# Optimization experiments

Measured on AMD Instinct MI355X. Metric: run time of the kernel, lower is better.

Reference implementation:

```python
import jax, jax.numpy as jnp
import numpy as np

B, T, C, H = 4, 2048, 2048, 16
D = C // H  # head dim = 128


def setup_inputs() -> dict:
    key = jax.random.key(0)
    k1, k2, k3, k4 = jax.random.split(key, 4)
    x = jax.random.normal(k1, (B, T, C), dtype=jnp.float32)
    # per-token key mask; force token 0 valid so no causal row is fully masked
    tok_mask = jax.random.randint(k2, (B, T), 0, 2).astype(bool).at[:, 0].set(True)
    s = 1.0 / np.sqrt(C).astype(np.float32)
    W_qkv = jax.random.normal(k3, (C, 3 * C), dtype=jnp.float32) * s
    W_proj = jax.random.normal(k4, (C, C), dtype=jnp.float32) * s
    return {"x": x, "tok_mask": tok_mask, "W_qkv": W_qkv, "W_proj": W_proj}


def reference(x, tok_mask, W_qkv, W_proj):
    Bx, Tx, Cx = x.shape
    qkv = x @ W_qkv                              # [B,T,3C]
    q, k, v = jnp.split(qkv, 3, axis=-1)
    q = q.reshape(Bx, Tx, H, D)
    k = k.reshape(Bx, Tx, H, D)
    v = v.reshape(Bx, Tx, H, D)
    scale = 1.0 / np.sqrt(D).astype(np.float32)
    scores = jnp.einsum('bqhd,bkhd->bhqk', q, k) * scale  # [B,H,T,T]
    causal = jnp.tril(jnp.ones((Tx, Tx), dtype=bool))      # [T,T]
    # tok_mask broadcasts over the query dim (key mask), AND-ed with causal
    mask = tok_mask[:, None, :] & causal                   # [B,T,T]
    scores = jnp.where(mask[:, None, :, :], scores, -jnp.inf)
    attn = jax.nn.softmax(scores, axis=-1)                 # dropout p=0 -> identity
    y = jnp.einsum('bhqk,bkhd->bqhd', attn, v).reshape(Bx, Tx, Cx)
    return y @ W_proj
```

## Files before the change

kernel.cpp:

```cpp
#include <hip/hip_runtime.h>
#include <hip/hip_bf16.h>
#include <stdint.h>

typedef __bf16 bf16;
typedef __bf16 bf16x8 __attribute__((ext_vector_type(8)));
typedef __bf16 bf16x4 __attribute__((ext_vector_type(4)));
typedef float f32x4 __attribute__((ext_vector_type(4)));
typedef unsigned short u16;
typedef unsigned int u32;

constexpr int NB = 4;
constexpr int NT = 2048;
constexpr int NC = 2048;
constexpr int NH = 16;
constexpr int ND = 128;
constexpr int NC3 = 6144;

__device__ __forceinline__ void gload16(const void* g, void* l) {
  __builtin_amdgcn_global_load_lds((const __attribute__((address_space(1))) void*)g,
                                   (__attribute__((address_space(3))) void*)l, 16, 0, 0);
}

__device__ __forceinline__ u32 pack_bf16(float a, float b) {
  return (u32)__builtin_bit_cast(u16, (bf16)a) | ((u32)__builtin_bit_cast(u16, (bf16)b) << 16);
}

__global__ __launch_bounds__(256) void ingest_k(const float* __restrict__ raw, bf16* __restrict__ out, long n) {
  long i = ((long)blockIdx.x * 256 + threadIdx.x) * 8;
  if (i >= n) return;
  f32x4 a = *(const f32x4*)(raw + i), b = *(const f32x4*)(raw + i + 4);
  bf16x8 o;
  o[0] = (bf16)a[0]; o[1] = (bf16)a[1]; o[2] = (bf16)a[2]; o[3] = (bf16)a[3];
  o[4] = (bf16)b[0]; o[5] = (bf16)b[1]; o[6] = (bf16)b[2]; o[7] = (bf16)b[3];
  *(bf16x8*)(out + i) = o;
}

__global__ void mask_prep_k(const void* raw, char* out) {
  __shared__ int s_gt1, s_oddnz, s_allb, s_allf, s_allh;
  if (threadIdx.x == 0) { s_gt1 = 0; s_oddnz = 0; s_allb = 1; s_allf = 1; s_allh = 1; }
  __syncthreads();
  const unsigned int* mw = (const unsigned int*)raw;
  int gt1 = 0, oddnz = 0, allb = 1, allf = 1, allh = 1;
  for (int i = threadIdx.x; i < 2048; i += 256) {
    unsigned v = mw[i];
    if (v > 1u) gt1 = 1;
    if ((i & 1) && v) oddnz = 1;
#pragma unroll
    for (int bb = 0; bb < 4; ++bb) { unsigned by = (v >> (8*bb)) & 0xffu; if (by > 1u) allb = 0; }
    if (v != 0u && v != 0x3F800000u) allf = 0;
    unsigned lo = v & 0xffffu, hi = v >> 16;
    if ((lo != 0u && lo != 0x3F80u) || (hi != 0u && hi != 0x3F80u)) allh = 0;
  }
  if (gt1) atomicOr(&s_gt1, 1);
  if (oddnz) atomicOr(&s_oddnz, 1);
  if (!allb) atomicAnd(&s_allb, 0);
  if (!allf) atomicAnd(&s_allf, 0);
  if (!allh) atomicAnd(&s_allh, 0);
  __syncthreads();
  int mode;
  if (!s_gt1)       mode = s_oddnz ? 0 : 2;
  else if (s_allf)  mode = 3;
  else if (s_allb)  mode = 1;
  else if (s_allh)  mode = 4;
  else              mode = 0;
  for (int i = threadIdx.x; i < NB*NT; i += 256) {
    int v;
    if (mode == 0)      v = (((const int*)raw)[i] != 0);
    else if (mode == 1) v = (((const unsigned char*)raw)[i] != 0);
    else if (mode == 2) v = (((const long long*)raw)[i] != 0);
    else if (mode == 3) v = (((const unsigned int*)raw)[i] != 0);
    else                v = (((const unsigned short*)raw)[i] != 0);
    out[i] = (char)v;
  }
}

__global__ __launch_bounds__(256) void transpose_f32_k(const float* __restrict__ in, bf16* __restrict__ out,
                                                       int in_rs, int out_rs) {
  __shared__ __align__(16) bf16 t[64][72];
  const int r0 = blockIdx.y << 6, c0 = blockIdx.x << 6;
  const int tid = threadIdx.x;
#pragma unroll
  for (int i = 0; i < 4; ++i) {
    int slot = i*256 + tid, row = slot >> 4, c4 = slot & 15;
    f32x4 v = *(const f32x4*)(in + (long)(r0 + row)*in_rs + c0 + c4*4);
#pragma unroll
    for (int e = 0; e < 4; ++e) t[c4*4 + e][row] = (bf16)v[e];
  }
  __syncthreads();
#pragma unroll
  for (int i = 0; i < 2; ++i) {
    int slot = i*256 + tid, row = slot >> 3, c8 = slot & 7;
    bf16x8 v = *(const bf16x8*)(&t[row][c8*8]);
    *(bf16x8*)(out + (long)(c0 + row)*out_rs + r0 + c8*8) = v;
  }
}

#define G256_READ_A(qm_) \
  _Pragma("unroll") \
  for (int mi = 0; mi < 4; ++mi) { \
    _Pragma("unroll") \
    for (int kk = 0; kk < 2; ++kk) { \
      const int ri = (qm_)*64 + mi*16 + r; \
      af[mi*2+kk] = *(const bf16x8*)(Ac + wm*16384 + ri*128 + (((kk*4 + g) ^ (ri & 7)) << 4)); \
    } \
  }
#define G256_READ_B(qn_) \
  _Pragma("unroll") \
  for (int ni = 0; ni < 2; ++ni) { \
    _Pragma("unroll") \
    for (int kk = 0; kk < 2; ++kk) { \
      const int ri = (qn_)*32 + ni*16 + r; \
      bfr[ni*2+kk] = *(const bf16x8*)(Bc + wn*8192 + ri*128 + (((kk*4 + g) ^ (ri & 7)) << 4)); \
    } \
  }
#define G256_MFMA(mb_, nb_) \
  __builtin_amdgcn_s_setprio(1); \
  _Pragma("unroll") \
  for (int mi = 0; mi < 4; ++mi) \
    _Pragma("unroll") \
    for (int ni = 0; ni < 2; ++ni) \
      _Pragma("unroll") \
      for (int kk = 0; kk < 2; ++kk) \
        acc[(mb_)+mi][(nb_)+ni] = __builtin_amdgcn_mfma_f32_16x16x32_bf16(af[mi*2+kk], bfr[ni*2+kk], acc[(mb_)+mi][(nb_)+ni], 0, 0, 0); \
  __builtin_amdgcn_s_setprio(0);
#define G256_EDGE(vm_) \
  asm volatile("s_waitcnt vmcnt(" #vm_ ")" ::: "memory"); \
  __builtin_amdgcn_s_barrier(); \
  __builtin_amdgcn_sched_barrier(0);
#define G256_EDGE_NOVM() \
  asm volatile("" ::: "memory"); \
  __builtin_amdgcn_s_barrier(); \
  __builtin_amdgcn_sched_barrier(0);

template <typename OT, bool VTE>
__global__ __launch_bounds__(512, 2) void gemm256_k(const bf16* __restrict__ A, const bf16* __restrict__ BT,
                                                    OT* __restrict__ Cout, int M, int N, int K, int nbx) {
  const int nwg = gridDim.x;
  const int bid = blockIdx.x;
  const int cpx = nwg >> 3;
  const int swz = (bid & 7) * cpx + (bid >> 3);
  const int bx = swz % nbx, by = swz / nbx;
  const long m0 = (long)by << 8, n0 = (long)bx << 8;

  const int tid = threadIdx.x, w = tid >> 6, l = tid & 63, g = l >> 4, r = l & 15;
  const int wm = w >> 2, wn = w & 3;

  __shared__ __align__(16) char As[2][32768];
  __shared__ __align__(16) char Bs[2][32768];

  long aoff2[4], boff2[4];
  int alds[4], blds[4];
#pragma unroll
  for (int i = 0; i < 4; ++i) {
    int s = i*256 + (tid & 255);
    int ri = s >> 3, c = s & 7, cp = c ^ (ri & 7);
    aoff2[i] = (m0 + wm*128 + ri) * (long)K + cp*8;
    alds[i] = wm*16384 + ((i*256 + (w & 3)*64) << 4);
    int s2 = i*128 + wm*64 + l;
    int ri2 = s2 >> 3, c2 = s2 & 7, cp2 = c2 ^ (ri2 & 7);
    boff2[i] = (n0 + wn*64 + ri2) * (long)K + cp2*8;
    blds[i] = wn*8192 + ((i*128 + wm*64) << 4);
  }

  const f32x4 z4 = {0.f, 0.f, 0.f, 0.f};
  f32x4 acc[8][4];
#pragma unroll
  for (int i = 0; i < 8; ++i)
#pragma unroll
    for (int j = 0; j < 4; ++j) acc[i][j] = z4;

  const int nk = K >> 6;
  gload16(A + aoff2[0], As[0] + alds[0]);
  gload16(A + aoff2[1], As[0] + alds[1]);
  gload16(BT + boff2[0], Bs[0] + blds[0]);
  gload16(BT + boff2[1], Bs[0] + blds[1]);
  gload16(A + aoff2[2], As[0] + alds[2]);
  gload16(A + aoff2[3], As[0] + alds[3]);
  gload16(BT + boff2[2], Bs[0] + blds[2]);
  gload16(BT + boff2[3], Bs[0] + blds[3]);
  G256_EDGE(4);

  bf16x8 af[8], bfr[4];

  for (int t = 0; t < nk - 1; ++t) {
    const int cur = t & 1;
    const char* Ac = As[cur];
    const char* Bc = Bs[cur];
    char* An = As[cur ^ 1];
    char* Bn = Bs[cur ^ 1];
    const long ko = (long)(t + 1) << 6;

    G256_READ_A(0); G256_READ_B(0);
    gload16(A + aoff2[0] + ko, An + alds[0]);
    gload16(A + aoff2[1] + ko, An + alds[1]);
    gload16(BT + boff2[0] + ko, Bn + blds[0]);
    gload16(BT + boff2[1] + ko, Bn + blds[1]);
    G256_MFMA(0, 0);
    G256_EDGE(6);

    G256_READ_A(1);
    gload16(A + aoff2[2] + ko, An + alds[2]);
    gload16(A + aoff2[3] + ko, An + alds[3]);
    gload16(BT + boff2[2] + ko, Bn + blds[2]);
    gload16(BT + boff2[3] + ko, Bn + blds[3]);
    G256_MFMA(4, 0);
    G256_EDGE(8);

    G256_READ_B(1);
    G256_MFMA(4, 2);
    G256_EDGE_NOVM();

    G256_READ_A(0);
    G256_MFMA(0, 2);
    G256_EDGE(4);
  }

  {
    const int cur = (nk - 1) & 1;
    const char* Ac = As[cur];
    const char* Bc = Bs[cur];
    G256_READ_A(0); G256_READ_B(0);
    G256_MFMA(0, 0);
    G256_EDGE(2);
    G256_READ_A(1);
    G256_MFMA(4, 0);
    G256_EDGE(0);
    G256_READ_B(1);
    G256_MFMA(4, 2);
    G256_EDGE_NOVM();
    G256_READ_A(0);
    G256_MFMA(0, 2);
  }

  if (VTE && n0 >= 2*NC) {
#pragma unroll
    for (int mi = 0; mi < 8; ++mi)
#pragma unroll
      for (int ni = 0; ni < 4; ++ni) {
        int d_f = (int)(n0 - 2*NC) + wn*64 + ni*16 + r;
        long mr = m0 + wm*128 + mi*16 + 4*g;
        int bb = (int)(mr >> 11), tt = (int)(mr & 2047);
        int hh = d_f >> 7, dd = d_f & 127;
        long rr = (long)(bb*NH + hh)*ND + dd;
        bf16x4 v;
        v[0] = (bf16)acc[mi][ni][0]; v[1] = (bf16)acc[mi][ni][1];
        v[2] = (bf16)acc[mi][ni][2]; v[3] = (bf16)acc[mi][ni][3];
        *(bf16x4*)(Cout + rr*NC3 + 2*NC + tt) = v;
      }
  } else {
#pragma unroll
    for (int mi = 0; mi < 8; ++mi)
#pragma unroll
      for (int ni = 0; ni < 4; ++ni)
#pragma unroll
        for (int j = 0; j < 4; ++j) {
          long mr = m0 + wm*128 + mi*16 + 4*g + j;
          long nc = n0 + wn*64 + ni*16 + r;
          Cout[mr*(long)N + nc] = (OT)acc[mi][ni][j];
        }
  }
}

__global__ __launch_bounds__(256, 2) void attn_k(const bf16* __restrict__ qkv,
                                                 const char* __restrict__ maskC, bf16* __restrict__ y) {
  const int qx = blockIdx.x, h = blockIdx.y, b = blockIdx.z;
  const int qb = (qx & 1) ? (15 - (qx >> 1)) : (qx >> 1);
  const int tid = threadIdx.x, w = tid >> 6, l = tid & 63, g = l >> 4, r = l & 15;
  const int q0 = qb << 7;
  const int bh = b*NH + h;
  const int ntiles = (qb << 1) + 2;
  const int qrowA = q0 + w*32 + r;
  const int qrowB = qrowA + 16;

  __shared__ __align__(16) char Klds[2][16384];
  __shared__ __align__(16) char Vlds[2][16384];
  __shared__ __align__(16) char Plds[8192];
  __shared__ char Mc[2048];
  char* Pl = Plds + (w << 11);

  for (int i = tid; i < q0 + 128; i += 256) Mc[i] = maskC[b*NT + i];

  long koff[4], voff[4];
  int klo[4];
#pragma unroll
  for (int i = 0; i < 4; ++i) {
    int slot = i*256 + tid;
    int row = slot >> 4, c = slot & 15, cp = c ^ (row & 7);
    koff[i] = (long)row*NC3 + cp*8;
    klo[i] = (i*256 + w*64) << 4;
    int vrow = slot >> 3, vc = slot & 7, vcp = vc ^ (vrow & 7);
    voff[i] = (long)vrow*NC3 + vcp*8;
  }
  const bf16* kbase0 = qkv + (long)(b*NT)*NC3 + (NC + h*ND);
  const bf16* vbase0 = qkv + (long)bh*ND*NC3 + 2*NC;

  bf16x8 qfA[4], qfB[4];
  {
    const bf16* qpA = qkv + (long)(b*NT + qrowA)*NC3 + h*ND + g*8;
    const bf16* qpB = qkv + (long)(b*NT + qrowB)*NC3 + h*ND + g*8;
#pragma unroll
    for (int dk = 0; dk < 4; ++dk) {
      qfA[dk] = *(const bf16x8*)(qpA + dk*32);
      qfB[dk] = *(const bf16x8*)(qpB + dk*32);
    }
  }

  const f32x4 z4 = {0.f, 0.f, 0.f, 0.f};
  f32x4 accA[8], accB[8];
#pragma unroll
  for (int i = 0; i < 8; ++i) { accA[i] = z4; accB[i] = z4; }
  float m_runA = 0.0f, l_runA = 0.0f;
  float m_runB = 0.0f, l_runB = 0.0f;

  const float SCL = 0.08838834764831845f * 1.4426950408889634f;

#pragma unroll
  for (int i = 0; i < 4; ++i) {
    gload16(kbase0 + koff[i], Klds[0] + klo[i]);
    gload16(vbase0 + voff[i], Vlds[0] + klo[i]);
  }
  __syncthreads();

  for (int kt = 0; kt < ntiles; ++kt) {
    const int cur = kt & 1;
    if (kt + 1 < ntiles) {
      const bf16* kb = kbase0 + (long)((kt+1)*64)*NC3;
      const bf16* vb = vbase0 + (kt+1)*64;
#pragma unroll
      for (int i = 0; i < 4; ++i) {
        gload16(kb + koff[i], Klds[cur^1] + klo[i]);
        gload16(vb + voff[i], Vlds[cur^1] + klo[i]);
      }
    }
    const char* Kl = Klds[cur];
    const char* Vl = Vlds[cur];
    const int key0 = kt*64;
    const bool actB = (key0 <= q0 + w*32 + 31);
    const bool actA = (key0 <= q0 + w*32 + 15);

    if (actB) {
      u32 mw_[4];
#pragma unroll
      for (int kc = 0; kc < 4; ++kc) mw_[kc] = *(const u32*)(Mc + key0 + kc*16 + 4*g);

      float tvA[4][4], tvB[4][4];
      __builtin_amdgcn_s_setprio(1);
#pragma unroll
      for (int kc = 0; kc < 4; ++kc) {
        const int krow = kc*16 + r;
        bf16x8 kf[4];
#pragma unroll
        for (int dk = 0; dk < 4; ++dk)
          kf[dk] = *(const bf16x8*)(Kl + krow*256 + (((dk*4 + g) ^ (krow & 7)) << 4));
        f32x4 sB = z4;
#pragma unroll
        for (int dk = 0; dk < 4; ++dk)
          sB = __builtin_amdgcn_mfma_f32_16x16x32_bf16(kf[dk], qfB[dk], sB, 0, 0, 0);
        f32x4 sA = z4;
        if (actA) {
#pragma unroll
          for (int dk = 0; dk < 4; ++dk)
            sA = __builtin_amdgcn_mfma_f32_16x16x32_bf16(kf[dk], qfA[dk], sA, 0, 0, 0);
        }
#pragma unroll
        for (int j = 0; j < 4; ++j) {
          const int key = key0 + kc*16 + 4*g + j;
          const bool km = ((mw_[kc] >> (8*j)) & 0xffu) != 0;
          tvB[kc][j] = (km && key <= qrowB) ? sB[j]*SCL : -3.0e38f;
          tvA[kc][j] = (km && key <= qrowA) ? sA[j]*SCL : -3.0e38f;
        }
      }
      __builtin_amdgcn_s_setprio(0);

      bf16x8 paA[2], paB[2];
      if (actA) {
        float tmax = -3.0e38f;
#pragma unroll
        for (int kc = 0; kc < 4; ++kc)
#pragma unroll
          for (int j = 0; j < 4; ++j) tmax = fmaxf(tmax, tvA[kc][j]);
        tmax = fmaxf(tmax, __shfl_xor(tmax, 16));
        tmax = fmaxf(tmax, __shfl_xor(tmax, 32));
        if (!__all(tmax <= m_runA + 8.0f)) {
          float mn = fmaxf(m_runA, tmax);
          float al = exp2f(m_runA - mn);
          m_runA = mn;
          l_runA *= al;
          float alj[4];
#pragma unroll
          for (int j = 0; j < 4; ++j) alj[j] = __shfl(al, 4*g + j);
#pragma unroll
          for (int d0 = 0; d0 < 8; ++d0)
#pragma unroll
            for (int j = 0; j < 4; ++j) accA[d0][j] *= alj[j];
        }
        float rs = 0.f;
#pragma unroll
        for (int kc = 0; kc < 4; ++kc) {
          float p0 = exp2f(tvA[kc][0] - m_runA), p1 = exp2f(tvA[kc][1] - m_runA);
          float p2 = exp2f(tvA[kc][2] - m_runA), p3 = exp2f(tvA[kc][3] - m_runA);
          rs += (p0 + p1) + (p2 + p3);
          const int off = (kc*32 + g*8) ^ ((r & 7) << 4);
          uint2 wv; wv.x = pack_bf16(p0, p1); wv.y = pack_bf16(p2, p3);
          *(uint2*)(Pl + r*128 + off) = wv;
        }
        rs += __shfl_xor(rs, 16);
        rs += __shfl_xor(rs, 32);
        l_runA += rs;
        asm volatile("s_waitcnt lgkmcnt(0)" ::: "memory");
        __builtin_amdgcn_sched_barrier(0);
#pragma unroll
        for (int kk = 0; kk < 2; ++kk)
          paA[kk] = *(const bf16x8*)(Pl + r*128 + ((kk*64 + g*16) ^ ((r & 7) << 4)));
        asm volatile("s_waitcnt lgkmcnt(0)" ::: "memory");
        __builtin_amdgcn_sched_barrier(0);
      }
      {
        float tmax = -3.0e38f;
#pragma unroll
        for (int kc = 0; kc < 4; ++kc)
#pragma unroll
          for (int j = 0; j < 4; ++j) tmax = fmaxf(tmax, tvB[kc][j]);
        tmax = fmaxf(tmax, __shfl_xor(tmax, 16));
        tmax = fmaxf(tmax, __shfl_xor(tmax, 32));
        if (!__all(tmax <= m_runB + 8.0f)) {
          float mn = fmaxf(m_runB, tmax);
          float al = exp2f(m_runB - mn);
          m_runB = mn;
          l_runB *= al;
          float alj[4];
#pragma unroll
          for (int j = 0; j < 4; ++j) alj[j] = __shfl(al, 4*g + j);
#pragma unroll
          for (int d0 = 0; d0 < 8; ++d0)
#pragma unroll
            for (int j = 0; j < 4; ++j) accB[d0][j] *= alj[j];
        }
        float rs = 0.f;
#pragma unroll
        for (int kc = 0; kc < 4; ++kc) {
          float p0 = exp2f(tvB[kc][0] - m_runB), p1 = exp2f(tvB[kc][1] - m_runB);
          float p2 = exp2f(tvB[kc][2] - m_runB), p3 = exp2f(tvB[kc][3] - m_runB);
          rs += (p0 + p1) + (p2 + p3);
          const int off = (kc*32 + g*8) ^ ((r & 7) << 4);
          uint2 wv; wv.x = pack_bf16(p0, p1); wv.y = pack_bf16(p2, p3);
          *(uint2*)(Pl + r*128 + off) = wv;
        }
        rs += __shfl_xor(rs, 16);
        rs += __shfl_xor(rs, 32);
        l_runB += rs;
        asm volatile("s_waitcnt lgkmcnt(0)" ::: "memory");
        __builtin_amdgcn_sched_barrier(0);
#pragma unroll
        for (int kk = 0; kk < 2; ++kk)
          paB[kk] = *(const bf16x8*)(Pl + r*128 + ((kk*64 + g*16) ^ ((r & 7) << 4)));
      }

      __builtin_amdgcn_s_setprio(1);
#pragma unroll
      for (int d0 = 0; d0 < 8; ++d0) {
        const int vrow = d0*16 + r;
#pragma unroll
        for (int kk = 0; kk < 2; ++kk) {
          bf16x8 vf = *(const bf16x8*)(Vl + vrow*128 + (((kk*4 + g) ^ (vrow & 7)) << 4));
          accB[d0] = __builtin_amdgcn_mfma_f32_16x16x32_bf16(paB[kk], vf, accB[d0], 0, 0, 0);
          if (actA) accA[d0] = __builtin_amdgcn_mfma_f32_16x16x32_bf16(paA[kk], vf, accA[d0], 0, 0, 0);
        }
      }
      __builtin_amdgcn_s_setprio(0);
    }
    __syncthreads();
  }

  {
    float lrA[4], lrB[4];
#pragma unroll
    for (int j = 0; j < 4; ++j) {
      lrA[j] = __shfl(l_runA, 4*g + j);
      lrB[j] = __shfl(l_runB, 4*g + j);
    }
#pragma unroll
    for (int d0 = 0; d0 < 8; ++d0)
#pragma unroll
      for (int j = 0; j < 4; ++j) {
        int qrA = q0 + w*32 + 4*g + j;
        y[(long)(b*NT + qrA)*NC + h*ND + d0*16 + r] = (bf16)(accA[d0][j] / lrA[j]);
        y[(long)(b*NT + qrA + 16)*NC + h*ND + d0*16 + r] = (bf16)(accB[d0][j] / lrB[j]);
      }
  }
}

extern "C" void kernel_launch(void* const* d_in, const int* in_sizes, int n_in,
                              void* d_out, int out_size, void* d_ws, size_t ws_size,
                              hipStream_t stream) {
  const float* xr     = (const float*)d_in[0];
  const void*  tok    = d_in[1];
  const float* wqkvr  = (const float*)d_in[2];
  const float* wprojr = (const float*)d_in[3];
  float* out = (float*)d_out;
  char* ws = (char*)d_ws;

  bf16* qkv    = (bf16*)(ws);
  bf16* yattn  = (bf16*)(ws + 100663296L);
  bf16* wT     = (bf16*)(ws + 134217728L);
  bf16* wpT    = (bf16*)(ws + 159383552L);
  bf16* xb     = (bf16*)(ws + 167772160L);
  char* maskC  = (char*)(ws + 201326592L);

  mask_prep_k<<<1, 256, 0, stream>>>(tok, maskC);
  ingest_k<<<8192, 256, 0, stream>>>(xr, xb, 16777216L);
  transpose_f32_k<<<dim3(96, 32), 256, 0, stream>>>(wqkvr, wT, NC3, NC);
  transpose_f32_k<<<dim3(32, 32), 256, 0, stream>>>(wprojr, wpT, NC, NC);
  gemm256_k<bf16, true><<<768, 512, 0, stream>>>(xb, wT, qkv, 8192, 6144, 2048, 24);
  attn_k<<<dim3(16, 16, 4), 256, 0, stream>>>(qkv, maskC, yattn);
  gemm256_k<float, false><<<256, 512, 0, stream>>>(yattn, wpT, out, 8192, 2048, 2048, 8);
}
```

Baseline: 533.5 us.

## Merge prep kernels into one launch and single-buffer attention K/V for occupancy

The mask conversion, input cast and two weight transposes now run as one launch, with work chosen by block index, which removes three kernel launches. Separately, the attention kernel drops K/V double buffering to cut LDS use and raises its launch bound to three blocks per SM. Each tile's load now finishes before compute starts, so global loads are no longer overlapped with MFMA work. The hoped-for gain from extra occupancy has to outweigh that lost overlap, and the lower register budget risks spills.

```diff
diff --git a/kernel.cpp b/kernel.cpp
--- a/kernel.cpp
+++ b/kernel.cpp
@@ -25,73 +25,77 @@
   return (u32)__builtin_bit_cast(u16, (bf16)a) | ((u32)__builtin_bit_cast(u16, (bf16)b) << 16);
 }
 
-__global__ __launch_bounds__(256) void ingest_k(const float* __restrict__ raw, bf16* __restrict__ out, long n) {
-  long i = ((long)blockIdx.x * 256 + threadIdx.x) * 8;
-  if (i >= n) return;
-  f32x4 a = *(const f32x4*)(raw + i), b = *(const f32x4*)(raw + i + 4);
-  bf16x8 o;
-  o[0] = (bf16)a[0]; o[1] = (bf16)a[1]; o[2] = (bf16)a[2]; o[3] = (bf16)a[3];
-  o[4] = (bf16)b[0]; o[5] = (bf16)b[1]; o[6] = (bf16)b[2]; o[7] = (bf16)b[3];
-  *(bf16x8*)(out + i) = o;
-}
-
-__global__ void mask_prep_k(const void* raw, char* out) {
+__global__ __launch_bounds__(256) void prep_k(const void* tok, char* maskC,
+                                              const float* __restrict__ xr, bf16* __restrict__ xb,
+                                              const float* __restrict__ wqkvr, bf16* __restrict__ wT,
+                                              const float* __restrict__ wprojr, bf16* __restrict__ wpT) {
+  __shared__ __align__(16) bf16 t[64][72];
   __shared__ int s_gt1, s_oddnz, s_allb, s_allf, s_allh;
-  if (threadIdx.x == 0) { s_gt1 = 0; s_oddnz = 0; s_allb = 1; s_allf = 1; s_allh = 1; }
-  __syncthreads();
-  const unsigned int* mw = (const unsigned int*)raw;
-  int gt1 = 0, oddnz = 0, allb = 1, allf = 1, allh = 1;
-  for (int i = threadIdx.x; i < 2048; i += 256) {
-    unsigned v = mw[i];
-    if (v > 1u) gt1 = 1;
-    if ((i & 1) && v) oddnz = 1;
-#pragma unroll
-    for (int bb = 0; bb < 4; ++bb) { unsigned by = (v >> (8*bb)) & 0xffu; if (by > 1u) allb = 0; }
-    if (v != 0u && v != 0x3F800000u) allf = 0;
-    unsigned lo = v & 0xffffu, hi = v >> 16;
-    if ((lo != 0u && lo != 0x3F80u) || (hi != 0u && hi != 0x3F80u)) allh = 0;
-  }
-  if (gt1) atomicOr(&s_gt1, 1);
-  if (oddnz) atomicOr(&s_oddnz, 1);
-  if (!allb) atomicAnd(&s_allb, 0);
-  if (!allf) atomicAnd(&s_allf, 0);
-  if (!allh) atomicAnd(&s_allh, 0);
-  __syncthreads();
-  int mode;
-  if (!s_gt1)       mode = s_oddnz ? 0 : 2;
-  else if (s_allf)  mode = 3;
-  else if (s_allb)  mode = 1;
-  else if (s_allh)  mode = 4;
-  else              mode = 0;
-  for (int i = threadIdx.x; i < NB*NT; i += 256) {
-    int v;
-    if (mode == 0)      v = (((const int*)raw)[i] != 0);
-    else if (mode == 1) v = (((const unsigned char*)raw)[i] != 0);
-    else if (mode == 2) v = (((const long long*)raw)[i] != 0);
-    else if (mode == 3) v = (((const unsigned int*)raw)[i] != 0);
-    else                v = (((const unsigned short*)raw)[i] != 0);
-    out[i] = (char)v;
-  }
-}
-
-__global__ __launch_bounds__(256) void transpose_f32_k(const float* __restrict__ in, bf16* __restrict__ out,
-                                                       int in_rs, int out_rs) {
-  __shared__ __align__(16) bf16 t[64][72];
-  const int r0 = blockIdx.y << 6, c0 = blockIdx.x << 6;
+  const int gid = blockIdx.x;
   const int tid = threadIdx.x;
-#pragma unroll
-  for (int i = 0; i < 4; ++i) {
-    int slot = i*256 + tid, row = slot >> 4, c4 = slot & 15;
-    f32x4 v = *(const f32x4*)(in + (long)(r0 + row)*in_rs + c0 + c4*4);
-#pragma unroll
-    for (int e = 0; e < 4; ++e) t[c4*4 + e][row] = (bf16)v[e];
-  }
-  __syncthreads();
-#pragma unroll
-  for (int i = 0; i < 2; ++i) {
-    int slot = i*256 + tid, row = slot >> 3, c8 = slot & 7;
-    bf16x8 v = *(const bf16x8*)(&t[row][c8*8]);
-    *(bf16x8*)(out + (long)(c0 + row)*out_rs + r0 + c8*8) = v;
+
+  if (gid == 0) {
+    if (tid == 0) { s_gt1 = 0; s_oddnz = 0; s_allb = 1; s_allf = 1; s_allh = 1; }
+    __syncthreads();
+    const unsigned int* mw = (const unsigned int*)tok;
+    int gt1 = 0, oddnz = 0, allb = 1, allf = 1, allh = 1;
+    for (int i = tid; i < 2048; i += 256) {
+      unsigned v = mw[i];
+      if (v > 1u) gt1 = 1;
+      if ((i & 1) && v) oddnz = 1;
+#pragma unroll
+      for (int bb = 0; bb < 4; ++bb) { unsigned by = (v >> (8*bb)) & 0xffu; if (by > 1u) allb = 0; }
+      if (v != 0u && v != 0x3F800000u) allf = 0;
+      unsigned lo = v & 0xffffu, hi = v >> 16;
+      if ((lo != 0u && lo != 0x3F80u) || (hi != 0u && hi != 0x3F80u)) allh = 0;
+    }
+    if (gt1) atomicOr(&s_gt1, 1);
+    if (oddnz) atomicOr(&s_oddnz, 1);
+    if (!allb) atomicAnd(&s_allb, 0);
+    if (!allf) atomicAnd(&s_allf, 0);
+    if (!allh) atomicAnd(&s_allh, 0);
+    __syncthreads();
+    int mode;
+    if (!s_gt1)       mode = s_oddnz ? 0 : 2;
+    else if (s_allf)  mode = 3;
+    else if (s_allb)  mode = 1;
+    else if (s_allh)  mode = 4;
+    else              mode = 0;
+    for (int i = tid; i < NB*NT; i += 256) {
+      int v;
+      if (mode == 0)      v = (((const int*)tok)[i] != 0);
+      else if (mode == 1) v = (((const unsigned char*)tok)[i] != 0);
+      else if (mode == 2) v = (((const long long*)tok)[i] != 0);
+      else if (mode == 3) v = (((const unsigned int*)tok)[i] != 0);
+      else                v = (((const unsigned short*)tok)[i] != 0);
+      maskC[i] = (char)v;
+    }
+  } else if (gid < 8193) {
+    long i = ((long)(gid - 1) * 256 + tid) * 8;
+    f32x4 a = *(const f32x4*)(xr + i), b = *(const f32x4*)(xr + i + 4);
+    bf16x8 o;
+    o[0] = (bf16)a[0]; o[1] = (bf16)a[1]; o[2] = (bf16)a[2]; o[3] = (bf16)a[3];
+    o[4] = (bf16)b[0]; o[5] = (bf16)b[1]; o[6] = (bf16)b[2]; o[7] = (bf16)b[3];
+    *(bf16x8*)(xb + i) = o;
+  } else {
+    const float* in; bf16* out; int in_rs, out_rs, bx, by;
+    if (gid < 11265) { int idx = gid - 8193; in = wqkvr; out = wT;  in_rs = NC3; out_rs = NC; bx = idx % 96; by = idx / 96; }
+    else             { int idx = gid - 11265; in = wprojr; out = wpT; in_rs = NC;  out_rs = NC; bx = idx % 32; by = idx / 32; }
+    const int r0 = by << 6, c0 = bx << 6;
+#pragma unroll
+    for (int i = 0; i < 4; ++i) {
+      int slot = i*256 + tid, row = slot >> 4, c4 = slot & 15;
+      f32x4 v = *(const f32x4*)(in + (long)(r0 + row)*in_rs + c0 + c4*4);
+#pragma unroll
+      for (int e = 0; e < 4; ++e) t[c4*4 + e][row] = (bf16)v[e];
+    }
+    __syncthreads();
+#pragma unroll
+    for (int i = 0; i < 2; ++i) {
+      int slot = i*256 + tid, row = slot >> 3, c8 = slot & 7;
+      bf16x8 v = *(const bf16x8*)(&t[row][c8*8]);
+      *(bf16x8*)(out + (long)(c0 + row)*out_rs + r0 + c8*8) = v;
+    }
   }
 }
 
@@ -261,7 +265,7 @@
   }
 }
 
-__global__ __launch_bounds__(256, 2) void attn_k(const bf16* __restrict__ qkv,
+__global__ __launch_bounds__(256, 3) void attn_k(const bf16* __restrict__ qkv,
                                                  const char* __restrict__ maskC, bf16* __restrict__ y) {
   const int qx = blockIdx.x, h = blockIdx.y, b = blockIdx.z;
   const int qb = (qx & 1) ? (15 - (qx >> 1)) : (qx >> 1);
@@ -272,8 +276,8 @@
   const int qrowA = q0 + w*32 + r;
   const int qrowB = qrowA + 16;
 
-  __shared__ __align__(16) char Klds[2][16384];
-  __shared__ __align__(16) char Vlds[2][16384];
+  __shared__ __align__(16) char Klds[16384];
+  __shared__ __align__(16) char Vlds[16384];
   __shared__ __align__(16) char Plds[8192];
   __shared__ char Mc[2048];
   char* Pl = Plds + (w << 11);
@@ -314,27 +318,19 @@
 
   const float SCL = 0.08838834764831845f * 1.4426950408889634f;
 
-#pragma unroll
-  for (int i = 0; i < 4; ++i) {
-    gload16(kbase0 + koff[i], Klds[0] + klo[i]);
-    gload16(vbase0 + voff[i], Vlds[0] + klo[i]);
-  }
-  __syncthreads();
-
   for (int kt = 0; kt < ntiles; ++kt) {
-    const int cur = kt & 1;
-    if (kt + 1 < ntiles) {
-      const bf16* kb = kbase0 + (long)((kt+1)*64)*NC3;
-      const bf16* vb = vbase0 + (kt+1)*64;
+    const int key0 = kt*64;
+    {
+      const bf16* kb = kbase0 + (long)key0*NC3;
+      const bf16* vb = vbase0 + key0;
 #pragma unroll
       for (int i = 0; i < 4; ++i) {
-        gload16(kb + koff[i], Klds[cur^1] + klo[i]);
-        gload16(vb + voff[i], Vlds[cur^1] + klo[i]);
-      }
-    }
-    const char* Kl = Klds[cur];
-    const char* Vl = Vlds[cur];
-    const int key0 = kt*64;
+        gload16(kb + koff[i], Klds + klo[i]);
+        gload16(vb + voff[i], Vlds + klo[i]);
+      }
+    }
+    __syncthreads();
+
     const bool actB = (key0 <= q0 + w*32 + 31);
     const bool actA = (key0 <= q0 + w*32 + 15);
 
@@ -351,7 +347,7 @@
         bf16x8 kf[4];
 #pragma unroll
         for (int dk = 0; dk < 4; ++dk)
-          kf[dk] = *(const bf16x8*)(Kl + krow*256 + (((dk*4 + g) ^ (krow & 7)) << 4));
+          kf[dk] = *(const bf16x8*)(Klds + krow*256 + (((dk*4 + g) ^ (krow & 7)) << 4));
         f32x4 sB = z4;
 #pragma unroll
         for (int dk = 0; dk < 4; ++dk)
@@ -462,7 +458,7 @@
         const int vrow = d0*16 + r;
 #pragma unroll
         for (int kk = 0; kk < 2; ++kk) {
-          bf16x8 vf = *(const bf16x8*)(Vl + vrow*128 + (((kk*4 + g) ^ (vrow & 7)) << 4));
+          bf16x8 vf = *(const bf16x8*)(Vlds + vrow*128 + (((kk*4 + g) ^ (vrow & 7)) << 4));
           accB[d0] = __builtin_amdgcn_mfma_f32_16x16x32_bf16(paB[kk], vf, accB[d0], 0, 0, 0);
           if (actA) accA[d0] = __builtin_amdgcn_mfma_f32_16x16x32_bf16(paA[kk], vf, accA[d0], 0, 0, 0);
         }
@@ -507,10 +503,7 @@
   bf16* xb     = (bf16*)(ws + 167772160L);
   char* maskC  = (char*)(ws + 201326592L);
 
-  mask_prep_k<<<1, 256, 0, stream>>>(tok, maskC);
-  ingest_k<<<8192, 256, 0, stream>>>(xr, xb, 16777216L);
-  transpose_f32_k<<<dim3(96, 32), 256, 0, stream>>>(wqkvr, wT, NC3, NC);
-  transpose_f32_k<<<dim3(32, 32), 256, 0, stream>>>(wprojr, wpT, NC, NC);
+  prep_k<<<12289, 256, 0, stream>>>(tok, maskC, xr, xb, wqkvr, wT, wprojr, wpT);
   gemm256_k<bf16, true><<<768, 512, 0, stream>>>(xb, wT, qkv, 8192, 6144, 2048, 24);
   attn_k<<<dim3(16, 16, 4), 256, 0, stream>>>(qkv, maskC, yattn);
   gemm256_k<float, false><<<256, 512, 0, stream>>>(yattn, wpT, out, 8192, 2048, 2048, 8);
```

New measurement: 817.5 us. 1.53x slower.
